# Optimization experiments

Measured on AMD Instinct MI355X. Metric: run time of the kernel, lower is better.

The kernel has to match this reference:

```python
import jax, jax.numpy as jnp
import numpy as np

K = 16                       # target expected number of distinct classes
NUM_LEVELS = 128             # num_discretization_levels
EPSILON = 0.1                # smoothing for derivative scales
NEWTON_ITERS = 3


def compute_normalizer(probs, k):
    """Solve for alpha s.t. sum_i (1 - exp(-alpha * p_i)) == k via Newton."""
    n = probs.shape[-1]
    alpha = jnp.full(probs.shape[:-1], float(k), dtype=probs.dtype)
    for _ in range(NEWTON_ITERS):
        e = jnp.exp(-alpha[..., None] * probs)          # (*, N)
        err = e.sum(axis=-1) + (k - n)                   # (*,)
        minus_d = (e * probs).sum(axis=-1)               # (*,)
        alpha = alpha + err / minus_d
    return alpha


def _derivative_scales(probs, eps):
    inv_p1 = 0.5 / (probs + eps)
    inv_p2 = 0.5 / (1.0 + eps - probs)
    common = eps * (inv_p1 + inv_p2)
    return inv_p1 + common, inv_p2 + common


@jax.custom_vjp
def fake_parameterized_dropout(probs, values, mask):
    return values * mask


def _fpd_fwd(probs, values, mask):
    return values * mask, (probs, values, mask)


def _fpd_bwd(res, g):
    probs, values, mask = res
    mask_grad = g * values
    s1, s2 = _derivative_scales(probs, EPSILON)
    probs_grad = mask_grad * (s1 * mask + s2 * (1.0 - mask))
    values_grad = g * mask
    return probs_grad, values_grad, jnp.zeros_like(mask)


fake_parameterized_dropout.defvjp(_fpd_fwd, _fpd_bwd)


def setup_inputs() -> dict:
    key = jax.random.key(0)
    k1, k2, k3, k4 = jax.random.split(key, 4)
    B, S, N = 4, 4096, 512
    return {
        "logits": jax.random.normal(k1, (B, S, N), dtype=jnp.float32),
        "values": jax.random.normal(k2, (B, S, N), dtype=jnp.float32),
        "u_mask": jax.random.uniform(k3, (B, S, N), dtype=jnp.float32),
        "u_disc": jax.random.uniform(k4, (B, S, N), dtype=jnp.float32),
    }


def reference(logits, values, u_mask, u_disc):
    probs = jax.nn.softmax(logits, axis=-1)                      # (*, N)
    alpha = compute_normalizer(probs, K)                         # (*,)
    # marginal prob of each class being chosen in K rounds
    marginals = 1.0 - (1.0 - probs) ** alpha[..., None]          # (*, N)
    # stochastic discretization with straight-through gradient
    idx = jnp.floor(marginals * (NUM_LEVELS - 1) + u_disc)
    y = idx * (1.0 / (NUM_LEVELS - 1))
    y_st = marginals + jax.lax.stop_gradient(y - marginals)
    # sample 0/1 mask with marginal probabilities y_st
    mask = (u_mask < y_st).astype(values.dtype)
    out = fake_parameterized_dropout(y_st, values, mask)
    return out
```

## Files before the change

kernel.cpp:

```cpp
#include <hip/hip_runtime.h>
#include <math.h>


#define ROW_N 512
#define EPW 16
constexpr double LEVELS_M1 = 127.0;
constexpr double INV_LEVELS_M1 = 1.0 / 127.0;

typedef float v4f __attribute__((ext_vector_type(4)));

template <int CTRL>
__device__ __forceinline__ float dpp_f32(float v) {
    int x = __builtin_amdgcn_update_dpp(0, __float_as_int(v), CTRL, 0xF, 0xF, true);
    return __int_as_float(x);
}
template <int CTRL>
__device__ __forceinline__ double dpp_f64(double v) {
    long long b = __double_as_longlong(v);
    int lo = __builtin_amdgcn_update_dpp(0, (int)(b & 0xFFFFFFFFLL), CTRL, 0xF, 0xF, true);
    int hi = __builtin_amdgcn_update_dpp(0, (int)(b >> 32),          CTRL, 0xF, 0xF, true);
    return __longlong_as_double(((long long)hi << 32) | (unsigned int)(unsigned)lo);
}

__device__ __forceinline__ double half_sum_f64(double v) {
    v += dpp_f64<0xB1>(v);
    v += dpp_f64<0x4E>(v);
    v += dpp_f64<0x141>(v);
    v += dpp_f64<0x140>(v);
    v += __shfl_xor(v, 16, 64);
    return v;
}
__device__ __forceinline__ float half_sum_f32(float v) {
    v += dpp_f32<0xB1>(v);
    v += dpp_f32<0x4E>(v);
    v += dpp_f32<0x141>(v);
    v += dpp_f32<0x140>(v);
    v += __shfl_xor(v, 16, 64);
    return v;
}

__device__ __forceinline__ double fast_recip1(double d) {
    double y = (double)__builtin_amdgcn_rcpf((float)d);
    return y * fma(-d, y, 2.0);
}

template <int DEG>
__device__ __forceinline__ double fast_exp(double x) {
    constexpr double C[12] = {
        1.0, 1.0, 0.5,
        1.6666666666666666574e-01,
        4.1666666666666664354e-02,
        8.3333333333333332177e-03,
        1.3888888888888889419e-03,
        1.9841269841269841253e-04,
        2.4801587301587301566e-05,
        2.7557319223985892511e-06,
        2.7557319223985888276e-07,
        2.5052108385441718775e-08
    };
    const double LOG2E = 1.4426950408889634074;
    const double LN2   = 6.9314718055994530942e-01;
    double kd = rint(x * LOG2E);
    double r  = fma(-kd, LN2, x);
    double p = C[DEG];
    #pragma unroll
    for (int k = DEG - 1; k >= 0; --k) p = fma(p, r, C[k]);
    long long sb = ((long long)(1023 + (int)kd)) << 52;
    return p * __longlong_as_double(sb);
}

__device__ __forceinline__ double log1p_atanh(double r) {
    double u  = r * fast_recip1(2.0 + r);
    double u2 = u * u;
    double q = 2.0 / 9.0;
    q = fma(q, u2, 2.0 / 7.0);
    q = fma(q, u2, 2.0 / 5.0);
    q = fma(q, u2, 2.0 / 3.0);
    q = fma(q, u2, 2.0);
    return u * q;
}

__device__ __forceinline__ double log1p_small(double r) {
    double q = 1.0 / 7.0;
    q = fma(q, r, -1.0 / 6.0);
    q = fma(q, r,  1.0 / 5.0);
    q = fma(q, r, -1.0 / 4.0);
    q = fma(q, r,  1.0 / 3.0);
    q = fma(q, r, -1.0 / 2.0);
    q = fma(q, r,  1.0);
    return r * q;
}

__global__ __launch_bounds__(256)
void sbm_kernel(const float* __restrict__ logits,
                const float* __restrict__ values,
                const float* __restrict__ u_mask,
                const float* __restrict__ u_disc,
                float* __restrict__ out,
                int rows)
{
    const int wave = (int)((blockIdx.x * (unsigned)blockDim.x + threadIdx.x) >> 6);
    const int lane = (int)(threadIdx.x & 63u);
    if (2 * wave >= rows) return;

    const int half = lane >> 5;
    const int c    = lane & 31;
    const size_t pb = (size_t)wave * 256;
    const int    fi = half * 128 + c;

    const float4* l4 = (const float4*)logits + pb + fi;
    float4 lg[4];
    #pragma unroll
    for (int g = 0; g < 4; ++g) lg[g] = l4[g * 32];

    double p[EPW];
    double s = 0.0;
    #pragma unroll
    for (int g = 0; g < 4; ++g) {
        const float lf[4] = {lg[g].x, lg[g].y, lg[g].z, lg[g].w};
        #pragma unroll
        for (int j = 0; j < 4; ++j) {
            p[g * 4 + j] = fast_exp<7>((double)lf[j]);
            s += p[g * 4 + j];
        }
    }

    float4 vv[4], um[4], ud[4];
    {
        const float4* v4 = (const float4*)values + pb + fi;
        const float4* m4 = (const float4*)u_mask + pb + fi;
        const float4* d4 = (const float4*)u_disc + pb + fi;
        #pragma unroll
        for (int g = 0; g < 4; ++g) {
            vv[g] = v4[g * 32];
            um[g] = m4[g * 32];
            ud[g] = d4[g * 32];
        }
    }

    s = half_sum_f64(s);
    const double inv_s = fast_recip1(s);
    float p32[EPW];
    float pmax = 0.0f;
    #pragma unroll
    for (int i = 0; i < EPW; ++i) {
        p[i] *= inv_s;
        p32[i] = (float)p[i];
        pmax = fmaxf(pmax, p32[i]);
    }

    float se32 = 0.0f, sep32 = 0.0f;
    #pragma unroll
    for (int i = 0; i < EPW; ++i) {
        float e = __expf(-16.0f * p32[i]);
        se32 += e;
        sep32 = fmaf(e, p32[i], sep32);
    }
    se32  = half_sum_f32(se32);
    sep32 = half_sum_f32(sep32);
    const float a32 = 16.0f + (se32 - 496.0f) / sep32;

    double alpha = (double)a32;
    {
        double se = 0.0;
        float  sepf = 0.0f;
        #pragma unroll
        for (int i = 0; i < EPW; ++i) {
            double e = fast_exp<7>(-alpha * p[i]);
            se += e;
            sepf = fmaf((float)e, p32[i], sepf);
        }
        se   = half_sum_f64(se);
        sepf = half_sum_f32(sepf);
        alpha += (se - 496.0) * fast_recip1((double)sepf);
    }

    const bool big = __any(pmax > 0.04f);
    double L[EPW];
    if (!big) {
        #pragma unroll
        for (int i = 0; i < EPW; ++i) {
            const double t = 1.0 - p[i];
            L[i] = log1p_small(t - 1.0);
        }
    } else {
        #pragma unroll
        for (int i = 0; i < EPW; ++i) {
            const double t = 1.0 - p[i];
            L[i] = log1p_atanh(t - 1.0);
        }
    }

    v4f* o4 = (v4f*)out + pb + fi;
    #pragma unroll
    for (int g = 0; g < 4; ++g) {
        const float vf[4] = {vv[g].x, vv[g].y, vv[g].z, vv[g].w};
        const float uf[4] = {um[g].x, um[g].y, um[g].z, um[g].w};
        const float df[4] = {ud[g].x, ud[g].y, ud[g].z, ud[g].w};
        v4f of;
        #pragma unroll
        for (int j = 0; j < 4; ++j) {
            const int i = g * 4 + j;
            const double m = 1.0 - fast_exp<8>(alpha * L[i]);
            const double y = floor(fma(m, LEVELS_M1, (double)df[j])) * INV_LEVELS_M1;
            of[j] = ((double)uf[j] < y) ? vf[j] : 0.0f;
        }
        *(o4 + g * 32) = of;
    }
}

extern "C" void kernel_launch(void* const* d_in, const int* in_sizes, int n_in,
                              void* d_out, int out_size, void* d_ws, size_t ws_size,
                              hipStream_t stream) {
    const float* logits = (const float*)d_in[0];
    const float* values = (const float*)d_in[1];
    const float* u_mask = (const float*)d_in[2];
    const float* u_disc = (const float*)d_in[3];
    float* out = (float*)d_out;

    const int rows = in_sizes[0] / ROW_N;
    const int waves = rows / 2;
    const int block = 256;
    const int grid = (waves * 64 + block - 1) / block;

    sbm_kernel<<<grid, block, 0, stream>>>(logits, values, u_mask, u_disc, out, rows);
}
```

Measured before the change: 29.32 us.

## Reuse Newton exponentials to compute marginals algebraically in small-probability path

In the common small-probability path, the second Newton step's exp(-alpha1*p) values are kept and reused to form (1-p)^alpha2. This is done as E * exp(-v), with v built from a log1p series in p plus the alpha update, so one of the two per-element double exps becomes a short polynomial. The range-reduced exp in that path becomes a plain degree-11 Taylor polynomial, which relies on alpha*p staying small. This cuts fp64 arithmetic per element but leans on approximations that only hold for small probabilities, which the existing pmax guard is meant to enforce.

After: 31.57 us. +7.7%, slower.

```diff
diff --git a/kernel.cpp b/kernel.cpp
--- a/kernel.cpp
+++ b/kernel.cpp
@@ -44,29 +44,37 @@
     return y * fma(-d, y, 2.0);
 }
 
+constexpr double EXPC[12] = {
+    1.0, 1.0, 0.5,
+    1.6666666666666666574e-01,
+    4.1666666666666664354e-02,
+    8.3333333333333332177e-03,
+    1.3888888888888889419e-03,
+    1.9841269841269841253e-04,
+    2.4801587301587301566e-05,
+    2.7557319223985892511e-06,
+    2.7557319223985888276e-07,
+    2.5052108385441718775e-08
+};
+
 template <int DEG>
 __device__ __forceinline__ double fast_exp(double x) {
-    constexpr double C[12] = {
-        1.0, 1.0, 0.5,
-        1.6666666666666666574e-01,
-        4.1666666666666664354e-02,
-        8.3333333333333332177e-03,
-        1.3888888888888889419e-03,
-        1.9841269841269841253e-04,
-        2.4801587301587301566e-05,
-        2.7557319223985892511e-06,
-        2.7557319223985888276e-07,
-        2.5052108385441718775e-08
-    };
     const double LOG2E = 1.4426950408889634074;
     const double LN2   = 6.9314718055994530942e-01;
     double kd = rint(x * LOG2E);
     double r  = fma(-kd, LN2, x);
-    double p = C[DEG];
-    #pragma unroll
-    for (int k = DEG - 1; k >= 0; --k) p = fma(p, r, C[k]);
+    double p = EXPC[DEG];
+    #pragma unroll
+    for (int k = DEG - 1; k >= 0; --k) p = fma(p, r, EXPC[k]);
     long long sb = ((long long)(1023 + (int)kd)) << 52;
     return p * __longlong_as_double(sb);
+}
+
+__device__ __forceinline__ double poly_exp11(double x) {
+    double p = EXPC[11];
+    #pragma unroll
+    for (int k = 10; k >= 0; --k) p = fma(p, x, EXPC[k]);
+    return p;
 }
 
 __device__ __forceinline__ double log1p_atanh(double r) {
@@ -78,17 +86,6 @@
     q = fma(q, u2, 2.0 / 3.0);
     q = fma(q, u2, 2.0);
     return u * q;
-}
-
-__device__ __forceinline__ double log1p_small(double r) {
-    double q = 1.0 / 7.0;
-    q = fma(q, r, -1.0 / 6.0);
-    q = fma(q, r,  1.0 / 5.0);
-    q = fma(q, r, -1.0 / 4.0);
-    q = fma(q, r,  1.0 / 3.0);
-    q = fma(q, r, -1.0 / 2.0);
-    q = fma(q, r,  1.0);
-    return r * q;
 }
 
 __global__ __launch_bounds__(256)
@@ -158,54 +155,86 @@
     }
     se32  = half_sum_f32(se32);
     sep32 = half_sum_f32(sep32);
-    const float a32 = 16.0f + (se32 - 496.0f) / sep32;
-
-    double alpha = (double)a32;
-    {
+    const double alpha1 = (double)(16.0f + (se32 - 496.0f) / sep32);
+
+    const bool big = __any(pmax > 0.04f);
+    v4f* o4 = (v4f*)out + pb + fi;
+
+    if (!big) {
+        double E[EPW];
         double se = 0.0;
         float  sepf = 0.0f;
         #pragma unroll
         for (int i = 0; i < EPW; ++i) {
-            double e = fast_exp<7>(-alpha * p[i]);
-            se += e;
-            sepf = fmaf((float)e, p32[i], sepf);
+            E[i] = poly_exp11(-alpha1 * p[i]);
+            se += E[i];
+            sepf = fmaf((float)E[i], p32[i], sepf);
         }
         se   = half_sum_f64(se);
         sepf = half_sum_f32(sepf);
-        alpha += (se - 496.0) * fast_recip1((double)sepf);
-    }
-
-    const bool big = __any(pmax > 0.04f);
-    double L[EPW];
-    if (!big) {
-        #pragma unroll
-        for (int i = 0; i < EPW; ++i) {
-            const double t = 1.0 - p[i];
-            L[i] = log1p_small(t - 1.0);
+        const double upd = (se - 496.0) * fast_recip1((double)sepf);
+        const double alpha2 = alpha1 + upd;
+
+        #pragma unroll
+        for (int g = 0; g < 4; ++g) {
+            const float vf[4] = {vv[g].x, vv[g].y, vv[g].z, vv[g].w};
+            const float uf[4] = {um[g].x, um[g].y, um[g].z, um[g].w};
+            const float df[4] = {ud[g].x, ud[g].y, ud[g].z, ud[g].w};
+            v4f of;
+            #pragma unroll
+            for (int j = 0; j < 4; ++j) {
+                const int i = g * 4 + j;
+                const double pd = (double)p32[i];
+                double q = 1.0 / 7.0;
+                q = fma(q, pd, 1.0 / 6.0);
+                q = fma(q, pd, 1.0 / 5.0);
+                q = fma(q, pd, 1.0 / 4.0);
+                q = fma(q, pd, 1.0 / 3.0);
+                q = fma(q, pd, 1.0 / 2.0);
+                const double W = (pd * pd) * q;
+                const double v = fma(alpha2, W, upd * pd);
+                double gq = 1.0 / 24.0;
+                gq = fma(gq, v, -1.0 / 6.0);
+                gq = fma(gq, v,  0.5);
+                gq = fma(gq, v, -1.0);
+                gq = fma(gq, v,  1.0);
+                const double m = fma(-E[i], gq, 1.0);
+                const double y = floor(fma(m, LEVELS_M1, (double)df[j])) * INV_LEVELS_M1;
+                of[j] = ((double)uf[j] < y) ? vf[j] : 0.0f;
+            }
+            *(o4 + g * 32) = of;
         }
     } else {
-        #pragma unroll
-        for (int i = 0; i < EPW; ++i) {
-            const double t = 1.0 - p[i];
-            L[i] = log1p_atanh(t - 1.0);
-        }
-    }
-
-    v4f* o4 = (v4f*)out + pb + fi;
-    #pragma unroll
-    for (int g = 0; g < 4; ++g) {
-        const float vf[4] = {vv[g].x, vv[g].y, vv[g].z, vv[g].w};
-        const float uf[4] = {um[g].x, um[g].y, um[g].z, um[g].w};
-        const float df[4] = {ud[g].x, ud[g].y, ud[g].z, ud[g].w};
-        v4f of;
-        #pragma unroll
-        for (int j = 0; j < 4; ++j) {
-            const int i = g * 4 + j;
-            const double m = 1.0 - fast_exp<8>(alpha * L[i]);
-            const double y = floor(fma(m, LEVELS_M1, (double)df[j])) * INV_LEVELS_M1;
-            of[j] = ((double)uf[j] < y) ? vf[j] : 0.0f;
-        }
-        *(o4 + g * 32) = of;
+        double alpha = alpha1;
+        {
+            double se = 0.0;
+            float  sepf = 0.0f;
+            #pragma unroll
+            for (int i = 0; i < EPW; ++i) {
+                double e = fast_exp<7>(-alpha * p[i]);
+                se += e;
+                sepf = fmaf((float)e, p32[i], sepf);
+            }
+            se   = half_sum_f64(se);
+            sepf = half_sum_f32(sepf);
+            alpha += (se - 496.0) * fast_recip1((double)sepf);
+        }
+        #pragma unroll
+        for (int g = 0; g < 4; ++g) {
+            const float vf[4] = {vv[g].x, vv[g].y, vv[g].z, vv[g].w};
+            const float uf[4] = {um[g].x, um[g].y, um[g].z, um[g].w};
+            const float df[4] = {ud[g].x, ud[g].y, ud[g].z, ud[g].w};
+            v4f of;
+            #pragma unroll
+            for (int j = 0; j < 4; ++j) {
+                const int i = g * 4 + j;
+                const double L = log1p_atanh(-p[i]);
+                const double m = 1.0 - fast_exp<8>(alpha * L);
+                const double y = floor(fma(m, LEVELS_M1, (double)df[j])) * INV_LEVELS_M1;
+                of[j] = ((double)uf[j] < y) ? vf[j] : 0.0f;
+            }
+            *(o4 + g * 32) = of;
+        }
     }
 }
 
```
